# Kernel tuning notes

Hardware: AMD Instinct MI355X
Metric: run time of the kernel (lower is better)

Reference implementation:

```python
import jax, jax.numpy as jnp
import numpy as np
from jax.scipy.special import gammaln, digamma

V, H, K, B = 50000, 100, 50, 2048
BN_EPS = 1e-5
SAMPLE_KEY = jax.random.key(42)  # fixed key standing in for Dirichlet rsample noise


def setup_inputs() -> dict:
    key = jax.random.key(0)
    ks = jax.random.split(key, 6)
    def lin(k, fan_in, fan_out):
        bound = 1.0 / np.sqrt(fan_in)
        return jax.random.uniform(k, (fan_in, fan_out), jnp.float32, -bound, bound)
    return {
        'input_bows': jax.random.uniform(ks[0], (B, V), jnp.float32),  # BoW features
        'W1': lin(ks[1], V, H), 'b1': jnp.zeros((H,), jnp.float32),
        'W2': lin(ks[2], H, H), 'b2': jnp.zeros((H,), jnp.float32),
        'Wt': lin(ks[3], H, K), 'bt': jnp.zeros((K,), jnp.float32),
        'bn_gamma': jnp.ones((K,), jnp.float32), 'bn_beta': jnp.zeros((K,), jnp.float32),
        'Wd': lin(ks[4], K, V), 'bd': jnp.zeros((V,), jnp.float32),
    }


def reference(input_bows, W1, b1, W2, b2, Wt, bt, bn_gamma, bn_beta, Wd, bd):
    # --- MLP encoder: Linear -> Softplus, Linear -> Softplus ---
    h = jax.nn.softplus(input_bows @ W1 + b1)        # [B, H]
    h = jax.nn.softplus(h @ W2 + b2)                  # [B, H]
    # --- h2t: Linear -> BatchNorm1d (training-mode batch stats) -> exp ---
    t = h @ Wt + bt                                   # [B, K]
    mu = jnp.mean(t, axis=0)
    var = jnp.mean((t - mu) ** 2, axis=0)             # biased variance (torch BN)
    t_hat = (t - mu) * jax.lax.rsqrt(var + BN_EPS) * bn_gamma + bn_beta
    alpha = jnp.exp(t_hat)                            # Dirichlet concentration [B, K]
    # --- Dirichlet rsample: normalized Gamma (reparameterized) ---
    g = jax.random.gamma(SAMPLE_KEY, alpha)           # [B, K]
    sample = g / jnp.sum(g, axis=-1, keepdims=True)
    # --- decode: Linear -> log_softmax ---
    logits = jax.nn.log_softmax(sample @ Wd + bd, axis=-1)  # [B, V]
    rec_loss = -jnp.sum(logits * input_bows, axis=1)        # [B]
    # --- KL( Dirichlet(alpha) || Dirichlet(1) ) ---
    a0 = jnp.sum(alpha, axis=-1)                            # [B]
    kld = (gammaln(a0) - jnp.sum(gammaln(alpha), axis=-1) - gammaln(jnp.float32(K))
           + jnp.sum((alpha - 1.0) * (digamma(alpha) - digamma(a0)[:, None]), axis=-1))
    return sample, logits, kld, rec_loss
```

## Files before the change

kernel.cpp:

```cpp
#include <hip/hip_runtime.h>
#include <cstdint>
#include <cstddef>

#define DEV __device__ __forceinline__

struct TFKey { uint32_t a, b; };

DEV uint32_t rotl32(uint32_t x, uint32_t r){ return (x << r) | (x >> (32u - r)); }

DEV TFKey tf2x32(TFKey k, uint32_t x0, uint32_t x1){
  uint32_t ks0 = k.a, ks1 = k.b, ks2 = k.a ^ k.b ^ 0x1BD11BDAu;
  x0 += ks0; x1 += ks1;
  x0 += x1; x1 = rotl32(x1,13); x1 ^= x0;
  x0 += x1; x1 = rotl32(x1,15); x1 ^= x0;
  x0 += x1; x1 = rotl32(x1,26); x1 ^= x0;
  x0 += x1; x1 = rotl32(x1, 6); x1 ^= x0;
  x0 += ks1; x1 += ks2 + 1u;
  x0 += x1; x1 = rotl32(x1,17); x1 ^= x0;
  x0 += x1; x1 = rotl32(x1,29); x1 ^= x0;
  x0 += x1; x1 = rotl32(x1,16); x1 ^= x0;
  x0 += x1; x1 = rotl32(x1,24); x1 ^= x0;
  x0 += ks2; x1 += ks0 + 2u;
  x0 += x1; x1 = rotl32(x1,13); x1 ^= x0;
  x0 += x1; x1 = rotl32(x1,15); x1 ^= x0;
  x0 += x1; x1 = rotl32(x1,26); x1 ^= x0;
  x0 += x1; x1 = rotl32(x1, 6); x1 ^= x0;
  x0 += ks0; x1 += ks1 + 3u;
  x0 += x1; x1 = rotl32(x1,17); x1 ^= x0;
  x0 += x1; x1 = rotl32(x1,29); x1 ^= x0;
  x0 += x1; x1 = rotl32(x1,16); x1 ^= x0;
  x0 += x1; x1 = rotl32(x1,24); x1 ^= x0;
  x0 += ks1; x1 += ks2 + 4u;
  x0 += x1; x1 = rotl32(x1,13); x1 ^= x0;
  x0 += x1; x1 = rotl32(x1,15); x1 ^= x0;
  x0 += x1; x1 = rotl32(x1,26); x1 ^= x0;
  x0 += x1; x1 = rotl32(x1, 6); x1 ^= x0;
  x0 += ks2; x1 += ks0 + 5u;
  return TFKey{x0, x1};
}

DEV TFKey tf_child(TFKey k, uint32_t i){ return tf2x32(k, 0u, i); }
DEV uint32_t rb32(TFKey k){ TFKey o = tf2x32(k, 0u, 0u); return o.a ^ o.b; }

DEV float u01(TFKey k){
  uint32_t bits = rb32(k);
  return __uint_as_float((bits >> 9) | 0x3F800000u) - 1.0f;
}

DEV float cr_logf(float x){ return (float)log((double)x); }
DEV float cr_expf(float x){ return (float)exp((double)x); }
DEV float cr_powf(float x, float y){ return (float)pow((double)x, (double)y); }

DEV float xla_erfinv(float x){
  #pragma clang fp contract(off)
  float w = -(float)log1p((double)(-(x*x)));
  float p;
  if (w < 5.0f){
    w = w - 2.5f;
    p = 2.81022636e-08f;
    p = 3.43273939e-07f + p*w;
    p = -3.5233877e-06f + p*w;
    p = -4.39150654e-06f + p*w;
    p = 0.00021858087f  + p*w;
    p = -0.00125372503f + p*w;
    p = -0.00417768164f + p*w;
    p = 0.246640727f    + p*w;
    p = 1.50140941f     + p*w;
  } else {
    w = sqrtf(w) - 3.0f;
    p = -0.000200214257f;
    p = 0.000100950558f + p*w;
    p = 0.00134934322f  + p*w;
    p = -0.00367342844f + p*w;
    p = 0.00573950773f  + p*w;
    p = -0.0076224613f  + p*w;
    p = 0.00943887047f  + p*w;
    p = 1.00167406f     + p*w;
    p = 2.83297682f     + p*w;
  }
  return p*x;
}

DEV float normal_f(TFKey k){
  #pragma clang fp contract(off)
  uint32_t bits = rb32(k);
  float f = __uint_as_float((bits >> 9) | 0x3F800000u) - 1.0f;
  const float lo = -0x1.fffffep-1f;
  float u = f*2.0f + lo;
  u = fmaxf(lo, u);
  return 0x1.6a09e6p+0f * xla_erfinv(u);
}

DEV float gamma_one(TFKey ek, float alpha){
  #pragma clang fp contract(off)
  TFKey key = tf_child(ek, 0u);
  TFKey sub = tf_child(ek, 1u);
  bool bm = (alpha >= 1.0f);
  float a_orig = alpha;
  float ab = bm ? alpha : (alpha + 1.0f);
  const float c13 = 0x1.555556p-2f;
  float d = ab - c13;
  float c = c13 / sqrtf(d);
  float X = 0.0f, Vv = 1.0f, U = 2.0f;
  for (int it = 0; it < 1000; ++it){
    float sq = 1.0f - 0.0331f*(X*X);
    bool cont = false;
    if (U >= sq){
      float lV  = cr_logf(Vv);
      float rhs = 0.5f*X + ((d - d*Vv) + d*lV);
      cont = (cr_logf(U) >= rhs);
    }
    if (!cont) break;
    TFKey nk = tf_child(key, 0u);
    TFKey xk = tf_child(key, 1u);
    TFKey Uk = tf_child(key, 2u);
    key = nk;
    float x = 0.0f, v = -1.0f;
    for (int j = 0; j < 1000 && v <= 0.0f; ++j){
      TFKey nx = tf_child(xk, 0u);
      TFKey sk = tf_child(xk, 1u);
      xk = nx;
      x = normal_f(sk);
      v = 1.0f + x*c;
    }
    X = x*x;
    Vv = (v*v)*v;
    U = u01(Uk);
  }
  float boost = 1.0f;
  if (!bm) boost = cr_powf(u01(sub), 1.0f / a_orig);
  return (d*Vv)*boost;
}

DEV double digamma_d(double x){
  double r = 0.0;
  while (x < 6.0){ r -= 1.0/x; x += 1.0; }
  double ix = 1.0/x, ix2 = ix*ix;
  double ser = ix2*(1.0/12 - ix2*(1.0/120 - ix2*(1.0/252 - ix2*(1.0/240 - ix2*(1.0/132)))));
  return r + log(x) - 0.5*ix - ser;
}

DEV float softplus_cr(float x){
  double xd = (double)x;
  if (x > 0.0f) return (float)(xd + log1p(exp(-xd)));
  return (float)log1p(exp(xd));
}

__global__ __launch_bounds__(256) void k1_gemm(const float* __restrict__ bows,
                                               const float* __restrict__ W1,
                                               float* __restrict__ pre_part){
  __shared__ float At[4][16*80];
  int rowb = blockIdx.x * 64;
  int kb   = blockIdx.y * 400;
  int tid  = threadIdx.x;
  int w    = tid >> 6;
  int lane = tid & 63;
  int c    = lane & 31;
  int rh   = lane >> 5;
  int wrow = rowb + w*16;
  float acc[8][4] = {};
  int cols[4];
  #pragma unroll
  for (int j = 0; j < 4; ++j){ int col = c + 32*j; cols[j] = col < 100 ? col : 96; }
  float* mylds = At[w];
  for (int t = 0; t < 5; ++t){
    int k0 = kb + t*80;
    #pragma unroll
    for (int j = 0; j < 5; ++j){
      int idx = lane + 64*j;
      int r = idx / 20, kf = idx - 20*r;
      float4 v = *(const float4*)(bows + (size_t)(wrow + r)*50000 + k0 + kf*4);
      *(float4*)(mylds + idx*4) = v;
    }
    const float* wbase = W1 + (size_t)k0 * 100;
    #pragma unroll 2
    for (int k4 = 0; k4 < 80; k4 += 4){
      float wv[4][4];
      #pragma unroll
      for (int kk = 0; kk < 4; ++kk){
        const float* wr = wbase + (size_t)(k4 + kk)*100;
        #pragma unroll
        for (int j = 0; j < 4; ++j) wv[kk][j] = wr[cols[j]];
      }
      #pragma unroll
      for (int i = 0; i < 8; ++i){
        float4 a = *(const float4*)(mylds + (rh*8 + i)*80 + k4);
        #pragma unroll
        for (int kk = 0; kk < 4; ++kk){
          float av = (kk == 0) ? a.x : (kk == 1) ? a.y : (kk == 2) ? a.z : a.w;
          #pragma unroll
          for (int j = 0; j < 4; ++j) acc[i][j] = fmaf(av, wv[kk][j], acc[i][j]);
        }
      }
    }
  }
  float* pp = pre_part + (size_t)blockIdx.y * 204800;
  #pragma unroll
  for (int i = 0; i < 8; ++i)
    #pragma unroll
    for (int j = 0; j < 4; ++j){
      int col = c + 32*j;
      if (col < 100) pp[(size_t)(wrow + rh*8 + i)*100 + col] = acc[i][j];
    }
}

__global__ void k2a(const float* __restrict__ pre_part, const float* __restrict__ b1,
                    float* __restrict__ h1){
  int idx = blockIdx.x*256 + threadIdx.x;
  float s = 0.0f;
  #pragma unroll 5
  for (int sp = 0; sp < 125; ++sp) s += pre_part[(size_t)sp*204800 + idx];
  s += b1[idx % 100];
  h1[idx] = softplus_cr(s);
}

__global__ void k2b(const float* __restrict__ h1, const float* __restrict__ W2,
                    const float* __restrict__ b2, float* __restrict__ h2){
  int idx = blockIdx.x*256 + threadIdx.x;
  int row = idx / 100, c2 = idx - 100*row;
  float acc = 0.0f;
  for (int k = 0; k < 100; ++k) acc = fmaf(h1[row*100 + k], W2[k*100 + c2], acc);
  h2[idx] = softplus_cr(acc + b2[c2]);
}

__global__ void k2c(const float* __restrict__ h2, const float* __restrict__ Wt,
                    const float* __restrict__ bt, float* __restrict__ tbuf){
  int idx = blockIdx.x*256 + threadIdx.x;
  int row = idx / 50, c3 = idx - 50*row;
  float acc = 0.0f;
  for (int k = 0; k < 100; ++k) acc = fmaf(h2[row*100 + k], Wt[k*50 + c3], acc);
  tbuf[idx] = acc + bt[c3];
}

__global__ void k3_bn(const float* __restrict__ t, float* __restrict__ musig){
  int k = blockIdx.x, tid = threadIdx.x;
  __shared__ float red[256];
  float s = 0.0f;
  for (int r = tid; r < 2048; r += 256) s += t[r*50 + k];
  red[tid] = s; __syncthreads();
  for (int off = 128; off > 0; off >>= 1){ if (tid < off) red[tid] += red[tid+off]; __syncthreads(); }
  float mu = red[0] / 2048.0f;
  __syncthreads();
  float s2 = 0.0f;
  for (int r = tid; r < 2048; r += 256){ float d = t[r*50 + k] - mu; s2 += d*d; }
  red[tid] = s2; __syncthreads();
  for (int off = 128; off > 0; off >>= 1){ if (tid < off) red[tid] += red[tid+off]; __syncthreads(); }
  if (tid == 0){
    float var = red[0] / 2048.0f;
    musig[k] = mu;
    musig[64 + k] = (float)(1.0 / sqrt((double)(var + 1e-5f)));
  }
}

__global__ void k4_gamma(const float* __restrict__ t, const float* __restrict__ musig,
                         const float* __restrict__ bng, const float* __restrict__ bnb,
                         float* __restrict__ alpha_out, float* __restrict__ g_out){
  #pragma clang fp contract(off)
  int j = blockIdx.x*256 + threadIdx.x;
  int row = j / 50, k = j - 50*row; (void)row;
  float mu = musig[k], rs = musig[64 + k];
  float th = ((t[j] - mu) * rs) * bng[k] + bnb[k];
  float alpha = cr_expf(th);
  alpha_out[j] = alpha;
  TFKey master{0u, 42u};
  TFKey ek = tf2x32(master, 0u, (uint32_t)j);
  g_out[j] = gamma_one(ek, alpha);
}

__global__ void k5_row(const float* __restrict__ g, const float* __restrict__ alpha,
                       float* __restrict__ sample, float* __restrict__ kld){
  int lane = threadIdx.x & 63;
  int row = blockIdx.x*4 + (threadIdx.x >> 6);
  int base = row*50;
  float gv = (lane < 50) ? g[base + lane] : 0.0f;
  float av = (lane < 50) ? alpha[base + lane] : 0.0f;
  float sg = gv, a0 = av;
  for (int o = 32; o > 0; o >>= 1){ sg += __shfl_xor(sg, o, 64); a0 += __shfl_xor(a0, o, 64); }
  if (lane < 50) sample[base + lane] = gv / sg;
  double dga0 = digamma_d((double)a0);
  double gl = 0.0, tm = 0.0;
  if (lane < 50){
    double ad = (double)av;
    gl = lgamma(ad);
    tm = (ad - 1.0) * (digamma_d(ad) - dga0);
  }
  for (int o = 32; o > 0; o >>= 1){ gl += __shfl_xor(gl, o, 64); tm += __shfl_xor(tm, o, 64); }
  if (lane == 0)
    kld[row] = (float)(lgamma((double)a0) - gl - lgamma(50.0) + tm);
}

__global__ __launch_bounds__(256) void k6a(const float* __restrict__ sample,
                                           const float* __restrict__ Wd,
                                           const float* __restrict__ bd,
                                           const float* __restrict__ bows,
                                           double* __restrict__ part){
  __shared__ float s_lds[64*52];
  int rowb = blockIdx.x * 64;
  int colb = blockIdx.y * 256;
  int tid = threadIdx.x;
  for (int idx = tid; idx < 64*52; idx += 256){
    int r = idx / 52, k = idx - 52*r;
    s_lds[idx] = (k < 50) ? sample[(size_t)(rowb + r)*50 + k] : 0.0f;
  }
  __syncthreads();
  int lane = tid & 63, w = tid >> 6;
  int col = colb + 4*lane;
  bool act = col < 50000;
  float4 bd4 = {0.0f, 0.0f, 0.0f, 0.0f};
  if (act) bd4 = *(const float4*)(bd + col);
  for (int p = 0; p < 4; ++p){
    int r0 = w*16 + p*4;
    float4 acc[4] = {};
    const float* sb = s_lds + r0*52;
    if (act){
      #pragma unroll
      for (int q = 0; q < 12; ++q){
        #pragma unroll
        for (int kk = 0; kk < 4; ++kk){
          int k = q*4 + kk;
          float4 wd4 = *(const float4*)(Wd + (size_t)k*50000 + col);
          #pragma unroll
          for (int r = 0; r < 4; ++r){
            float sv = sb[r*52 + k];
            acc[r].x = fmaf(sv, wd4.x, acc[r].x);
            acc[r].y = fmaf(sv, wd4.y, acc[r].y);
            acc[r].z = fmaf(sv, wd4.z, acc[r].z);
            acc[r].w = fmaf(sv, wd4.w, acc[r].w);
          }
        }
      }
      #pragma unroll
      for (int kk = 0; kk < 2; ++kk){
        int k = 48 + kk;
        float4 wd4 = *(const float4*)(Wd + (size_t)k*50000 + col);
        #pragma unroll
        for (int r = 0; r < 4; ++r){
          float sv = sb[r*52 + k];
          acc[r].x = fmaf(sv, wd4.x, acc[r].x);
          acc[r].y = fmaf(sv, wd4.y, acc[r].y);
          acc[r].z = fmaf(sv, wd4.z, acc[r].z);
          acc[r].w = fmaf(sv, wd4.w, acc[r].w);
        }
      }
    }
    #pragma unroll
    for (int r = 0; r < 4; ++r){
      double se = 0.0, s1 = 0.0, sbw = 0.0;
      if (act){
        float4 bw = *(const float4*)(bows + (size_t)(rowb + r0 + r)*50000 + col);
        float zx = bd4.x + acc[r].x;
        float zy = bd4.y + acc[r].y;
        float zz = bd4.z + acc[r].z;
        float zw = bd4.w + acc[r].w;
        se  = ((double)expf(zx) + (double)expf(zy)) + ((double)expf(zz) + (double)expf(zw));
        s1  = (((double)zx*bw.x + (double)zy*bw.y) + ((double)zz*bw.z + (double)zw*bw.w));
        sbw = (((double)bw.x + (double)bw.y) + ((double)bw.z + (double)bw.w));
      }
      for (int o = 32; o > 0; o >>= 1){
        se  += __shfl_xor(se,  o, 64);
        s1  += __shfl_xor(s1,  o, 64);
        sbw += __shfl_xor(sbw, o, 64);
      }
      if (lane == 0){
        size_t off = ((size_t)(rowb + r0 + r)*196 + blockIdx.y)*3;
        part[off] = se; part[off+1] = s1; part[off+2] = sbw;
      }
    }
  }
}

__global__ void k6m(const double* __restrict__ part, float* __restrict__ lse,
                    float* __restrict__ rec){
  int row = blockIdx.x*256 + threadIdx.x;
  double se = 0, s1 = 0, sb = 0;
  const double* p = part + (size_t)row*588;
  for (int q = 0; q < 196; ++q){ se += p[3*q]; s1 += p[3*q+1]; sb += p[3*q+2]; }
  double l = log(se);
  lse[row] = (float)l;
  rec[row] = (float)(l*sb - s1);
}

__global__ __launch_bounds__(256) void k6b(const float* __restrict__ sample,
                                           const float* __restrict__ Wd,
                                           const float* __restrict__ bd,
                                           const float* __restrict__ lse,
                                           float* __restrict__ logits){
  __shared__ float s_lds[64*52];
  int rowb = blockIdx.x * 64;
  int colb = blockIdx.y * 256;
  int tid = threadIdx.x;
  for (int idx = tid; idx < 64*52; idx += 256){
    int r = idx / 52, k = idx - 52*r;
    s_lds[idx] = (k < 50) ? sample[(size_t)(rowb + r)*50 + k] : 0.0f;
  }
  __syncthreads();
  int lane = tid & 63, w = tid >> 6;
  int col = colb + 4*lane;
  bool act = col < 50000;
  float4 bd4 = {0.0f, 0.0f, 0.0f, 0.0f};
  if (act) bd4 = *(const float4*)(bd + col);
  for (int p = 0; p < 4; ++p){
    int r0 = w*16 + p*4;
    float4 acc[4] = {};
    const float* sb = s_lds + r0*52;
    if (act){
      #pragma unroll
      for (int q = 0; q < 12; ++q){
        #pragma unroll
        for (int kk = 0; kk < 4; ++kk){
          int k = q*4 + kk;
          float4 wd4 = *(const float4*)(Wd + (size_t)k*50000 + col);
          #pragma unroll
          for (int r = 0; r < 4; ++r){
            float sv = sb[r*52 + k];
            acc[r].x = fmaf(sv, wd4.x, acc[r].x);
            acc[r].y = fmaf(sv, wd4.y, acc[r].y);
            acc[r].z = fmaf(sv, wd4.z, acc[r].z);
            acc[r].w = fmaf(sv, wd4.w, acc[r].w);
          }
        }
      }
      #pragma unroll
      for (int kk = 0; kk < 2; ++kk){
        int k = 48 + kk;
        float4 wd4 = *(const float4*)(Wd + (size_t)k*50000 + col);
        #pragma unroll
        for (int r = 0; r < 4; ++r){
          float sv = sb[r*52 + k];
          acc[r].x = fmaf(sv, wd4.x, acc[r].x);
          acc[r].y = fmaf(sv, wd4.y, acc[r].y);
          acc[r].z = fmaf(sv, wd4.z, acc[r].z);
          acc[r].w = fmaf(sv, wd4.w, acc[r].w);
        }
      }
      #pragma unroll
      for (int r = 0; r < 4; ++r){
        float lf = lse[rowb + r0 + r];
        float4 z;
        z.x = (bd4.x + acc[r].x) - lf;
        z.y = (bd4.y + acc[r].y) - lf;
        z.z = (bd4.z + acc[r].z) - lf;
        z.w = (bd4.w + acc[r].w) - lf;
        *(float4*)(logits + (size_t)(rowb + r0 + r)*50000 + col) = z;
      }
    }
  }
}

extern "C" void kernel_launch(void* const* d_in, const int* in_sizes, int n_in,
                              void* d_out, int out_size, void* d_ws, size_t ws_size,
                              hipStream_t stream){
  (void)in_sizes; (void)n_in; (void)out_size; (void)ws_size;
  const float* bows = (const float*)d_in[0];
  const float* W1   = (const float*)d_in[1];
  const float* b1   = (const float*)d_in[2];
  const float* W2   = (const float*)d_in[3];
  const float* b2   = (const float*)d_in[4];
  const float* Wt   = (const float*)d_in[5];
  const float* bt   = (const float*)d_in[6];
  const float* bng  = (const float*)d_in[7];
  const float* bnb  = (const float*)d_in[8];
  const float* Wd   = (const float*)d_in[9];
  const float* bd   = (const float*)d_in[10];

  float* out    = (float*)d_out;
  float* sample = out;
  float* logits = out + 102400;
  float* kld    = out + 102400 + (size_t)2048*50000;
  float* rec    = kld + 2048;

  float*  pre_part = logits;
  float*  h1    = pre_part + (size_t)125*2048*100;
  float*  h2    = h1 + 204800;
  float*  tbuf  = h2 + 204800;
  float*  abuf  = tbuf + 102400;
  float*  gbuf  = abuf + 102400;
  float*  musig = gbuf + 102400;
  double* part  = (double*)(musig + 128);
  float*  lsew  = (float*)d_ws;

  k1_gemm<<<dim3(32, 125), 256, 0, stream>>>(bows, W1, pre_part);
  k2a<<<800, 256, 0, stream>>>(pre_part, b1, h1);
  k2b<<<800, 256, 0, stream>>>(h1, W2, b2, h2);
  k2c<<<400, 256, 0, stream>>>(h2, Wt, bt, tbuf);
  k3_bn<<<50, 256, 0, stream>>>(tbuf, musig);
  k4_gamma<<<400, 256, 0, stream>>>(tbuf, musig, bng, bnb, abuf, gbuf);
  k5_row<<<512, 256, 0, stream>>>(gbuf, abuf, sample, kld);
  k6a<<<dim3(32, 196), 256, 0, stream>>>(sample, Wd, bd, bows, part);
  k6m<<<8, 256, 0, stream>>>(part, lsew, rec);
  k6b<<<dim3(32, 196), 256, 0, stream>>>(sample, Wd, bd, lsew, logits);
}
```

Measured before the change: 1.133 ms.

## Register-tile 16 rows per wave in decoder kernels and read sample via scalar loads

The decoder GEMM kernels (k6a and k6b) now accumulate 16 rows per wave in registers instead of making four passes of 4 rows. Each Wd float4 is therefore loaded once per k rather than four times. The shared-memory staging of sample and its __syncthreads are removed: the wave index goes through readfirstlane, so sample values become wave-uniform scalar loads from global memory. The cost is 64 VGPRs of accumulators, which raises register pressure and may lower occupancy.

```diff
diff --git a/kernel.cpp b/kernel.cpp
--- a/kernel.cpp
+++ b/kernel.cpp
@@ -289,82 +289,60 @@
     kld[row] = (float)(lgamma((double)a0) - gl - lgamma(50.0) + tm);
 }
 
+
 __global__ __launch_bounds__(256) void k6a(const float* __restrict__ sample,
                                            const float* __restrict__ Wd,
                                            const float* __restrict__ bd,
                                            const float* __restrict__ bows,
                                            double* __restrict__ part){
-  __shared__ float s_lds[64*52];
-  int rowb = blockIdx.x * 64;
+  int tid = threadIdx.x;
+  int lane = tid & 63;
+  int w = __builtin_amdgcn_readfirstlane(tid >> 6);
+  int rowb = blockIdx.x * 64 + w*16;
   int colb = blockIdx.y * 256;
-  int tid = threadIdx.x;
-  for (int idx = tid; idx < 64*52; idx += 256){
-    int r = idx / 52, k = idx - 52*r;
-    s_lds[idx] = (k < 50) ? sample[(size_t)(rowb + r)*50 + k] : 0.0f;
-  }
-  __syncthreads();
-  int lane = tid & 63, w = tid >> 6;
   int col = colb + 4*lane;
   bool act = col < 50000;
   float4 bd4 = {0.0f, 0.0f, 0.0f, 0.0f};
   if (act) bd4 = *(const float4*)(bd + col);
-  for (int p = 0; p < 4; ++p){
-    int r0 = w*16 + p*4;
-    float4 acc[4] = {};
-    const float* sb = s_lds + r0*52;
+  const float* srow = sample + (size_t)rowb*50;
+  float4 acc[16];
+  #pragma unroll
+  for (int r = 0; r < 16; ++r){ acc[r].x = 0.0f; acc[r].y = 0.0f; acc[r].z = 0.0f; acc[r].w = 0.0f; }
+  if (act){
+    #pragma unroll 5
+    for (int k = 0; k < 50; ++k){
+      float4 wd4 = *(const float4*)(Wd + (size_t)k*50000 + col);
+      #pragma unroll
+      for (int r = 0; r < 16; ++r){
+        float sv = srow[r*50 + k];
+        acc[r].x = fmaf(sv, wd4.x, acc[r].x);
+        acc[r].y = fmaf(sv, wd4.y, acc[r].y);
+        acc[r].z = fmaf(sv, wd4.z, acc[r].z);
+        acc[r].w = fmaf(sv, wd4.w, acc[r].w);
+      }
+    }
+  }
+  #pragma unroll 2
+  for (int r = 0; r < 16; ++r){
+    double se = 0.0, s1 = 0.0, sbw = 0.0;
     if (act){
-      #pragma unroll
-      for (int q = 0; q < 12; ++q){
-        #pragma unroll
-        for (int kk = 0; kk < 4; ++kk){
-          int k = q*4 + kk;
-          float4 wd4 = *(const float4*)(Wd + (size_t)k*50000 + col);
-          #pragma unroll
-          for (int r = 0; r < 4; ++r){
-            float sv = sb[r*52 + k];
-            acc[r].x = fmaf(sv, wd4.x, acc[r].x);
-            acc[r].y = fmaf(sv, wd4.y, acc[r].y);
-            acc[r].z = fmaf(sv, wd4.z, acc[r].z);
-            acc[r].w = fmaf(sv, wd4.w, acc[r].w);
-          }
-        }
-      }
-      #pragma unroll
-      for (int kk = 0; kk < 2; ++kk){
-        int k = 48 + kk;
-        float4 wd4 = *(const float4*)(Wd + (size_t)k*50000 + col);
-        #pragma unroll
-        for (int r = 0; r < 4; ++r){
-          float sv = sb[r*52 + k];
-          acc[r].x = fmaf(sv, wd4.x, acc[r].x);
-          acc[r].y = fmaf(sv, wd4.y, acc[r].y);
-          acc[r].z = fmaf(sv, wd4.z, acc[r].z);
-          acc[r].w = fmaf(sv, wd4.w, acc[r].w);
-        }
-      }
-    }
-    #pragma unroll
-    for (int r = 0; r < 4; ++r){
-      double se = 0.0, s1 = 0.0, sbw = 0.0;
-      if (act){
-        float4 bw = *(const float4*)(bows + (size_t)(rowb + r0 + r)*50000 + col);
-        float zx = bd4.x + acc[r].x;
-        float zy = bd4.y + acc[r].y;
-        float zz = bd4.z + acc[r].z;
-        float zw = bd4.w + acc[r].w;
-        se  = ((double)expf(zx) + (double)expf(zy)) + ((double)expf(zz) + (double)expf(zw));
-        s1  = (((double)zx*bw.x + (double)zy*bw.y) + ((double)zz*bw.z + (double)zw*bw.w));
-        sbw = (((double)bw.x + (double)bw.y) + ((double)bw.z + (double)bw.w));
-      }
-      for (int o = 32; o > 0; o >>= 1){
-        se  += __shfl_xor(se,  o, 64);
-        s1  += __shfl_xor(s1,  o, 64);
-        sbw += __shfl_xor(sbw, o, 64);
-      }
-      if (lane == 0){
-        size_t off = ((size_t)(rowb + r0 + r)*196 + blockIdx.y)*3;
-        part[off] = se; part[off+1] = s1; part[off+2] = sbw;
-      }
+      float4 bw = *(const float4*)(bows + (size_t)(rowb + r)*50000 + col);
+      float zx = bd4.x + acc[r].x;
+      float zy = bd4.y + acc[r].y;
+      float zz = bd4.z + acc[r].z;
+      float zw = bd4.w + acc[r].w;
+      se  = ((double)expf(zx) + (double)expf(zy)) + ((double)expf(zz) + (double)expf(zw));
+      s1  = (((double)zx*bw.x + (double)zy*bw.y) + ((double)zz*bw.z + (double)zw*bw.w));
+      sbw = (((double)bw.x + (double)bw.y) + ((double)bw.z + (double)bw.w));
+    }
+    for (int o = 32; o > 0; o >>= 1){
+      se  += __shfl_xor(se,  o, 64);
+      s1  += __shfl_xor(s1,  o, 64);
+      sbw += __shfl_xor(sbw, o, 64);
+    }
+    if (lane == 0){
+      size_t off = ((size_t)(rowb + r)*196 + blockIdx.y)*3;
+      part[off] = se; part[off+1] = s1; part[off+2] = sbw;
     }
   }
 }
@@ -385,64 +363,41 @@
                                            const float* __restrict__ bd,
                                            const float* __restrict__ lse,
                                            float* __restrict__ logits){
-  __shared__ float s_lds[64*52];
-  int rowb = blockIdx.x * 64;
+  int tid = threadIdx.x;
+  int lane = tid & 63;
+  int w = __builtin_amdgcn_readfirstlane(tid >> 6);
+  int rowb = blockIdx.x * 64 + w*16;
   int colb = blockIdx.y * 256;
-  int tid = threadIdx.x;
-  for (int idx = tid; idx < 64*52; idx += 256){
-    int r = idx / 52, k = idx - 52*r;
-    s_lds[idx] = (k < 50) ? sample[(size_t)(rowb + r)*50 + k] : 0.0f;
-  }
-  __syncthreads();
-  int lane = tid & 63, w = tid >> 6;
   int col = colb + 4*lane;
   bool act = col < 50000;
   float4 bd4 = {0.0f, 0.0f, 0.0f, 0.0f};
   if (act) bd4 = *(const float4*)(bd + col);
-  for (int p = 0; p < 4; ++p){
-    int r0 = w*16 + p*4;
-    float4 acc[4] = {};
-    const float* sb = s_lds + r0*52;
-    if (act){
+  const float* srow = sample + (size_t)rowb*50;
+  float4 acc[16];
+  #pragma unroll
+  for (int r = 0; r < 16; ++r){ acc[r].x = 0.0f; acc[r].y = 0.0f; acc[r].z = 0.0f; acc[r].w = 0.0f; }
+  if (act){
+    #pragma unroll 5
+    for (int k = 0; k < 50; ++k){
+      float4 wd4 = *(const float4*)(Wd + (size_t)k*50000 + col);
       #pragma unroll
-      for (int q = 0; q < 12; ++q){
-        #pragma unroll
-        for (int kk = 0; kk < 4; ++kk){
-          int k = q*4 + kk;
-          float4 wd4 = *(const float4*)(Wd + (size_t)k*50000 + col);
-          #pragma unroll
-          for (int r = 0; r < 4; ++r){
-            float sv = sb[r*52 + k];
-            acc[r].x = fmaf(sv, wd4.x, acc[r].x);
-            acc[r].y = fmaf(sv, wd4.y, acc[r].y);
-            acc[r].z = fmaf(sv, wd4.z, acc[r].z);
-            acc[r].w = fmaf(sv, wd4.w, acc[r].w);
-          }
-        }
+      for (int r = 0; r < 16; ++r){
+        float sv = srow[r*50 + k];
+        acc[r].x = fmaf(sv, wd4.x, acc[r].x);
+        acc[r].y = fmaf(sv, wd4.y, acc[r].y);
+        acc[r].z = fmaf(sv, wd4.z, acc[r].z);
+        acc[r].w = fmaf(sv, wd4.w, acc[r].w);
       }
-      #pragma unroll
-      for (int kk = 0; kk < 2; ++kk){
-        int k = 48 + kk;
-        float4 wd4 = *(const float4*)(Wd + (size_t)k*50000 + col);
-        #pragma unroll
-        for (int r = 0; r < 4; ++r){
-          float sv = sb[r*52 + k];
-          acc[r].x = fmaf(sv, wd4.x, acc[r].x);
-          acc[r].y = fmaf(sv, wd4.y, acc[r].y);
-          acc[r].z = fmaf(sv, wd4.z, acc[r].z);
-          acc[r].w = fmaf(sv, wd4.w, acc[r].w);
-        }
-      }
-      #pragma unroll
-      for (int r = 0; r < 4; ++r){
-        float lf = lse[rowb + r0 + r];
-        float4 z;
-        z.x = (bd4.x + acc[r].x) - lf;
-        z.y = (bd4.y + acc[r].y) - lf;
-        z.z = (bd4.z + acc[r].z) - lf;
-        z.w = (bd4.w + acc[r].w) - lf;
-        *(float4*)(logits + (size_t)(rowb + r0 + r)*50000 + col) = z;
-      }
+    }
+    #pragma unroll 4
+    for (int r = 0; r < 16; ++r){
+      float lf = lse[rowb + r];
+      float4 z;
+      z.x = (bd4.x + acc[r].x) - lf;
+      z.y = (bd4.y + acc[r].y) - lf;
+      z.z = (bd4.z + acc[r].z) - lf;
+      z.w = (bd4.w + acc[r].w) - lf;
+      *(float4*)(logits + (size_t)(rowb + r)*50000 + col) = z;
     }
   }
 }
```

Result: slower. 1.331 ms (+17.5%).
